# Kernel optimization log

Hardware: AMD Instinct MI355X
Metric: run time of the kernel (lower is better)

Reference implementation:

```python
import jax, jax.numpy as jnp
import numpy as np

WINDOW = 10


def setup_inputs() -> dict:
    key = jax.random.key(0)
    k_r, k_w1, k_b1, k_w2, k_b2 = jax.random.split(key, 5)
    B, T = 2048, 4096
    returns = jax.random.normal(k_r, (B, T), dtype=jnp.float32)
    # nn.Linear default init ~ U(-1/sqrt(fan_in), 1/sqrt(fan_in)); scaled normals are fine for a reference
    W1 = jax.random.normal(k_w1, (32, WINDOW), dtype=jnp.float32) / np.sqrt(WINDOW)
    b1 = jax.random.normal(k_b1, (32,), dtype=jnp.float32) * 0.01
    W2 = jax.random.normal(k_w2, (1, 32), dtype=jnp.float32) / np.sqrt(32)
    b2 = jax.random.normal(k_b2, (1,), dtype=jnp.float32) * 0.01
    return {"returns": returns, "W1": W1, "b1": b1, "W2": W2, "b2": b2}


def reference(returns, W1, b1, W2, b2) -> jnp.ndarray:
    B, T = returns.shape
    w = WINDOW
    # Gather all sliding windows at once: window i covers returns[:, i:i+w] and
    # produces the estimate for timestep t = i + w (matching the torch loop).
    idx = jnp.arange(T - w)[:, None] + jnp.arange(w)[None, :]  # [T-w, w]
    wins = returns[:, idx]  # [B, T-w, w]
    h1 = jax.nn.relu(jnp.einsum('btw,hw->bth', wins, W1) + b1)  # [B, T-w, 32]
    h = 0.5 * jax.nn.sigmoid(jnp.einsum('bth,oh->bto', h1, W2) + b2)[..., 0]  # [B, T-w]
    # H[:, :window] = H[:, window] (the first computed value)
    head = jnp.broadcast_to(h[:, :1], (B, w))
    return jnp.concatenate([head, h], axis=1)  # [B, T]
```

## Files before the change

kernel.cpp:

```cpp
#include <hip/hip_runtime.h>

#define WINDOW 10
#define TDIM 4096
#define TVALID (TDIM - WINDOW)

typedef __attribute__((ext_vector_type(8)))  short bf16x8;
typedef __attribute__((ext_vector_type(8)))  __bf16 bfv8;
typedef __attribute__((ext_vector_type(8)))  float f32x8;
typedef __attribute__((ext_vector_type(16))) float f32x16;
typedef __attribute__((ext_vector_type(2)))  float f32x2;
typedef float f32x4u __attribute__((ext_vector_type(4), aligned(4)));

static __device__ __forceinline__ short f2bf(float f) {
  return (short)__builtin_bit_cast(unsigned short, (__bf16)f);
}

static __device__ __forceinline__ bf16x8 cvt8(const float* __restrict__ p, bool g1) {
  f32x4u a = *(const f32x4u*)p;
  f32x4u b = *(const f32x4u*)(p + 4);
  f32x8 f;
  f[0] = a[0]; f[1] = a[1]; f[2] = g1 ? 1.0f : a[2]; f[3] = a[3];
  f[4] = b[0]; f[5] = b[1]; f[6] = b[2]; f[7] = b[3];
  return __builtin_bit_cast(bf16x8, __builtin_convertvector(f, bfv8));
}

static __device__ __forceinline__ bf16x8 cvt8_clamp(const float* __restrict__ rowp,
                                                    int base, bool g1) {
  f32x8 f;
  #pragma unroll
  for (int j = 0; j < 8; ++j) {
    int idx = base + j; idx = idx < TDIM - 1 ? idx : TDIM - 1;
    f[j] = rowp[idx];
  }
  f[2] = g1 ? 1.0f : f[2];
  return __builtin_bit_cast(bf16x8, __builtin_convertvector(f, bfv8));
}

static __device__ __forceinline__ float l2dot(const f32x16& acc, const f32x2* __restrict__ w2p) {
  const f32x2 z2 = {0.f, 0.f};
  f32x2 s0 = z2, s1 = z2;
  #pragma unroll
  for (int j = 0; j < 8; j += 2) {
    f32x2 a = {acc[2*j],     acc[2*j + 1]};
    f32x2 b = {acc[2*j + 2], acc[2*j + 3]};
    s0 = __builtin_elementwise_fma(__builtin_elementwise_max(a, z2), w2p[j],     s0);
    s1 = __builtin_elementwise_fma(__builtin_elementwise_max(b, z2), w2p[j + 1], s1);
  }
  f32x2 s = s0 + s1;
  return s[0] + s[1];
}

static __device__ __forceinline__ float half_sigmoid(float z) {
  float e = __expf(-z);
  return 0.5f * __frcp_rn(1.0f + e) ;
}

__global__ __launch_bounds__(256) void hurst_mfma3(
    const float* __restrict__ ret, const float* __restrict__ W1,
    const float* __restrict__ b1,  const float* __restrict__ W2,
    const float* __restrict__ b2,  float* __restrict__ out) {
  const int lid = threadIdx.x & 63;
  const int wv  = threadIdx.x >> 6;
  const int n   = lid & 31;
  const int g   = lid >> 5;
  const bool g1 = (g == 1);

  bf16x8 af;
  if (!g1) {
    #pragma unroll
    for (int j = 0; j < 8; ++j) af[j] = f2bf(W1[n * WINDOW + j]);
  } else {
    af[0] = f2bf(W1[n * WINDOW + 8]);
    af[1] = f2bf(W1[n * WINDOW + 9]);
    af[2] = f2bf(b1[n]);
    #pragma unroll
    for (int j = 3; j < 8; ++j) af[j] = 0;
  }

  f32x2 w2p[8];
  #pragma unroll
  for (int j = 0; j < 8; ++j) {
    w2p[j][0] = W2[((2*j)   & 3) + 8 * ((2*j)   >> 2) + 4 * g];
    w2p[j][1] = W2[((2*j+1) & 3) + 8 * ((2*j+1) >> 2) + 4 * g];
  }
  const float b2c = b2[0];

  const int row = blockIdx.x;
  const float* __restrict__ rowp = ret + (size_t)row * TDIM;
  float* __restrict__ orow = out + (size_t)row * TDIM;
  const int seg   = wv * 1024;
  const int lbase = n + 8 * g;
  const float* __restrict__ lanep = rowp + seg + lbase;

  float y;

#define BODY(I, CLAMPED, PRED)                                               \
  {                                                                          \
    const int t0 = seg + (I) * 64;                                           \
    bf16x8 bv0 = cvt8(lanep + (I) * 64, g1);                                 \
    bf16x8 bv1 = (CLAMPED) ? cvt8_clamp(rowp, t0 + 32 + lbase, g1)           \
                           : cvt8(lanep + (I) * 64 + 32, g1);                \
    f32x16 acc0 = {}, acc1 = {};                                             \
    acc0 = __builtin_amdgcn_mfma_f32_32x32x16_bf16(af, bv0, acc0, 0, 0, 0);  \
    acc1 = __builtin_amdgcn_mfma_f32_32x32x16_bf16(af, bv1, acc1, 0, 0, 0);  \
    float P0 = l2dot(acc0, w2p);                                             \
    float P1 = l2dot(acc1, w2p);                                             \
    P0 += __shfl_xor(P0, 32, 64);                                            \
    P1 += __shfl_xor(P1, 32, 64);                                            \
    const float q = (lid < 32) ? P0 : P1;                                    \
    y = half_sigmoid(q + b2c);                                               \
    const int t = t0 + lid;                                                  \
    if (!(PRED) || t < TVALID) orow[WINDOW + t] = y;                         \
  }

  BODY(0, false, false)
  if (wv == 0) {
    const float y0 = __shfl(y, 0, 64);
    if (lid < WINDOW) orow[lid] = y0;
  }

  #pragma unroll
  for (int i = 1; i < 15; ++i) BODY(i, false, false)

  if (wv < 3) {
    BODY(15, false, false)
  } else {
    BODY(15, true, true)
  }
#undef BODY
}

extern "C" void kernel_launch(void* const* d_in, const int* in_sizes, int n_in,
                              void* d_out, int out_size, void* d_ws, size_t ws_size,
                              hipStream_t stream) {
  const float* ret = (const float*)d_in[0];
  const float* W1  = (const float*)d_in[1];
  const float* b1  = (const float*)d_in[2];
  const float* W2  = (const float*)d_in[3];
  const float* b2  = (const float*)d_in[4];
  float* out = (float*)d_out;

  const int B = in_sizes[0] / TDIM;
  dim3 block(256);
  dim3 grid(B);
  hipLaunchKernelGGL(hurst_mfma3, grid, block, 0, stream,
                     ret, W1, b1, W2, b2, out);
}
```

Measured before the change: 42.49 us.

## Prefetch next window loads, use permlane32 swap and fast reciprocal

Splits loading from bf16 packing so the next pair of 8-float input chunks is loaded one iteration ahead and overlaps with the MFMA and layer-2 reduction of the current pair. It also replaces the two xor shuffles plus select with a single permlane32_swap when the builtin exists, and swaps the round-to-nearest reciprocal in the sigmoid for the hardware approximate rcp. The aim is to hide global-load latency and cut cross-lane and ALU overhead. The cost is more live registers, and the approximate reciprocal can shift results slightly.

```diff
diff --git a/kernel.cpp b/kernel.cpp
--- a/kernel.cpp
+++ b/kernel.cpp
@@ -15,23 +15,26 @@
   return (short)__builtin_bit_cast(unsigned short, (__bf16)f);
 }
 
-static __device__ __forceinline__ bf16x8 cvt8(const float* __restrict__ p, bool g1) {
+static __device__ __forceinline__ f32x8 ld8(const float* __restrict__ p) {
   f32x4u a = *(const f32x4u*)p;
   f32x4u b = *(const f32x4u*)(p + 4);
   f32x8 f;
-  f[0] = a[0]; f[1] = a[1]; f[2] = g1 ? 1.0f : a[2]; f[3] = a[3];
+  f[0] = a[0]; f[1] = a[1]; f[2] = a[2]; f[3] = a[3];
   f[4] = b[0]; f[5] = b[1]; f[6] = b[2]; f[7] = b[3];
-  return __builtin_bit_cast(bf16x8, __builtin_convertvector(f, bfv8));
+  return f;
 }
 
-static __device__ __forceinline__ bf16x8 cvt8_clamp(const float* __restrict__ rowp,
-                                                    int base, bool g1) {
+static __device__ __forceinline__ f32x8 ld8c(const float* __restrict__ rowp, int base) {
   f32x8 f;
   #pragma unroll
   for (int j = 0; j < 8; ++j) {
     int idx = base + j; idx = idx < TDIM - 1 ? idx : TDIM - 1;
     f[j] = rowp[idx];
   }
+  return f;
+}
+
+static __device__ __forceinline__ bf16x8 packbf(f32x8 f, bool g1) {
   f[2] = g1 ? 1.0f : f[2];
   return __builtin_bit_cast(bf16x8, __builtin_convertvector(f, bfv8));
 }
@@ -50,12 +53,28 @@
   return s[0] + s[1];
 }
 
+static __device__ __forceinline__ float combine_halves(float Pe, float Po, int lid) {
+#if __has_builtin(__builtin_amdgcn_permlane32_swap)
+  auto r = __builtin_amdgcn_permlane32_swap(
+      __builtin_bit_cast(unsigned, Pe), __builtin_bit_cast(unsigned, Po), false, false);
+  return __builtin_bit_cast(float, (unsigned)r[0]) + __builtin_bit_cast(float, (unsigned)r[1]);
+#else
+  Pe += __shfl_xor(Pe, 32, 64);
+  Po += __shfl_xor(Po, 32, 64);
+  return (lid < 32) ? Pe : Po;
+#endif
+}
+
 static __device__ __forceinline__ float half_sigmoid(float z) {
   float e = __expf(-z);
-  return 0.5f * __frcp_rn(1.0f + e) ;
+#if __has_builtin(__builtin_amdgcn_rcpf)
+  return 0.5f * __builtin_amdgcn_rcpf(1.0f + e);
+#else
+  return 0.5f / (1.0f + e);
+#endif
 }
 
-__global__ __launch_bounds__(256) void hurst_mfma3(
+__global__ __launch_bounds__(256) void hurst_mfma5(
     const float* __restrict__ ret, const float* __restrict__ W1,
     const float* __restrict__ b1,  const float* __restrict__ W2,
     const float* __restrict__ b2,  float* __restrict__ out) {
@@ -92,42 +111,56 @@
   const int lbase = n + 8 * g;
   const float* __restrict__ lanep = rowp + seg + lbase;
 
+  f32x8 fe = ld8(lanep);
+  f32x8 fo = ld8(lanep + 32);
   float y;
 
-#define BODY(I, CLAMPED, PRED)                                               \
-  {                                                                          \
-    const int t0 = seg + (I) * 64;                                           \
-    bf16x8 bv0 = cvt8(lanep + (I) * 64, g1);                                 \
-    bf16x8 bv1 = (CLAMPED) ? cvt8_clamp(rowp, t0 + 32 + lbase, g1)           \
-                           : cvt8(lanep + (I) * 64 + 32, g1);                \
-    f32x16 acc0 = {}, acc1 = {};                                             \
-    acc0 = __builtin_amdgcn_mfma_f32_32x32x16_bf16(af, bv0, acc0, 0, 0, 0);  \
-    acc1 = __builtin_amdgcn_mfma_f32_32x32x16_bf16(af, bv1, acc1, 0, 0, 0);  \
-    float P0 = l2dot(acc0, w2p);                                             \
-    float P1 = l2dot(acc1, w2p);                                             \
-    P0 += __shfl_xor(P0, 32, 64);                                            \
-    P1 += __shfl_xor(P1, 32, 64);                                            \
-    const float q = (lid < 32) ? P0 : P1;                                    \
-    y = half_sigmoid(q + b2c);                                               \
-    const int t = t0 + lid;                                                  \
-    if (!(PRED) || t < TVALID) orow[WINDOW + t] = y;                         \
+#define PAIR(P, PRE, MASK)                                                     \
+  {                                                                            \
+    bf16x8 bve = packbf(fe, g1);                                               \
+    f32x16 acce = {};                                                          \
+    acce = __builtin_amdgcn_mfma_f32_32x32x16_bf16(af, bve, acce, 0, 0, 0);    \
+    if (PRE) fe = ld8(lanep + (2*(P)+2) * 32);                                 \
+    float Pe = l2dot(acce, w2p);                                               \
+    bf16x8 bvo = packbf(fo, g1);                                               \
+    f32x16 acco = {};                                                          \
+    acco = __builtin_amdgcn_mfma_f32_32x32x16_bf16(af, bvo, acco, 0, 0, 0);    \
+    if (PRE) fo = ld8(lanep + (2*(P)+3) * 32);                                 \
+    float Po = l2dot(acco, w2p);                                               \
+    const float q = combine_halves(Pe, Po, lid);                               \
+    y = half_sigmoid(q + b2c);                                                 \
+    const int t = seg + (P) * 64 + lid;                                        \
+    if (!(MASK) || t < TVALID) orow[WINDOW + t] = y;                           \
   }
 
-  BODY(0, false, false)
+  PAIR(0, true, false)
   if (wv == 0) {
     const float y0 = __shfl(y, 0, 64);
     if (lid < WINDOW) orow[lid] = y0;
   }
 
   #pragma unroll
-  for (int i = 1; i < 15; ++i) BODY(i, false, false)
+  for (int p = 1; p <= 13; ++p) PAIR(p, true, false)
 
-  if (wv < 3) {
-    BODY(15, false, false)
-  } else {
-    BODY(15, true, true)
+  {
+    bf16x8 bve = packbf(fe, g1);
+    f32x16 acce = {};
+    acce = __builtin_amdgcn_mfma_f32_32x32x16_bf16(af, bve, acce, 0, 0, 0);
+    fe = ld8(lanep + 30 * 32);
+    float Pe = l2dot(acce, w2p);
+    bf16x8 bvo = packbf(fo, g1);
+    f32x16 acco = {};
+    acco = __builtin_amdgcn_mfma_f32_32x32x16_bf16(af, bvo, acco, 0, 0, 0);
+    if (wv == 3) fo = ld8c(rowp, seg + 31 * 32 + lbase);
+    else         fo = ld8(lanep + 31 * 32);
+    float Po = l2dot(acco, w2p);
+    const float q = combine_halves(Pe, Po, lid);
+    y = half_sigmoid(q + b2c);
+    orow[WINDOW + seg + 14 * 64 + lid] = y;
   }
-#undef BODY
+
+  PAIR(15, false, true)
+#undef PAIR
 }
 
 extern "C" void kernel_launch(void* const* d_in, const int* in_sizes, int n_in,
@@ -143,6 +176,6 @@
   const int B = in_sizes[0] / TDIM;
   dim3 block(256);
   dim3 grid(B);
-  hipLaunchKernelGGL(hurst_mfma3, grid, block, 0, stream,
+  hipLaunchKernelGGL(hurst_mfma5, grid, block, 0, stream,
                      ret, W1, b1, W2, b2, out);
 }
```

Result: slower. 44.98 us (+5.9%).
